# Kernel optimization log

Hardware: AMD Instinct MI355X
Metric: run time of the kernel (lower is better)

## Reference

```python
import jax, jax.numpy as jnp
import numpy as np

B, S, D, F, E = 2, 1024, 1024, 4096, 8

def setup_inputs() -> dict:
    key = jax.random.key(0)
    ks = jax.random.split(key, 4)
    s = 0.02
    return {
        "x": jax.random.normal(ks[0], (B, S, D), dtype=jnp.float32),
        "switch_w": jax.random.normal(ks[1], (D, E), dtype=jnp.float32) * s,
        "switch_b": jnp.zeros((E,), dtype=jnp.float32),
        "w1": jax.random.normal(ks[2], (E, D, F), dtype=jnp.float32) * s,
        "b1": jnp.zeros((E, F), dtype=jnp.float32),
        "w2": jax.random.normal(ks[3], (E, F, D), dtype=jnp.float32) * s,
        "b2": jnp.zeros((E, D), dtype=jnp.float32),
    }

def reference(x, switch_w, switch_b, w1, b1, w2, b2):
    b, s, d = x.shape
    xt = x.reshape(-1, d)                               # [T, D]
    logits = xt @ switch_w + switch_b                   # [T, E]
    route_prob = jax.nn.softmax(logits, axis=-1)        # [T, E]
    route_prob_max = jnp.max(route_prob, axis=-1)       # [T]
    routes = jnp.argmax(route_prob, axis=-1)            # [T] int
    onehot = jax.nn.one_hot(routes, E, dtype=xt.dtype)  # [T, E]
    counts = onehot.sum(axis=0)                         # tokens per expert (float, as in torch new_tensor)

    # top-1 dispatch: run each expert FFN, keep only its tokens via mask (drop_tokens=False -> no capacity drop)
    def body(acc, params):
        W1, B1, W2, B2, mask = params                   # mask: [T]
        y = jax.nn.relu(xt @ W1 + B1) @ W2 + B2         # [T, D]
        return acc + mask[:, None] * y, None

    out, _ = jax.lax.scan(body, jnp.zeros_like(xt), (w1, b1, w2, b2, onehot.T))
    out = out * route_prob_max[:, None]                 # is_scale_prob=True
    final_output = out.reshape(b, s, d)
    return final_output, counts, route_prob.sum(axis=0), 0, route_prob_max
```

## Files before the change

### kernel.cpp

```cpp
#include <hip/hip_runtime.h>
#include <stdint.h>

#define T_TOK 2048
#define D_DIM 1024
#define F_DIM 4096
#define E_NUM 8
#define RPMAX 4096
#define BK 64

typedef __attribute__((ext_vector_type(8))) short bfx8;
typedef __attribute__((ext_vector_type(4))) float fx4;

__device__ __forceinline__ unsigned short f2bf(float f) {
  union { float f; uint32_t u; } v; v.f = f;
  uint32_t u = v.u;
  u += 0x7FFFu + ((u >> 16) & 1u);
  return (unsigned short)(u >> 16);
}

__device__ __forceinline__ void load_lds16(const unsigned short* g, unsigned short* l) {
  __builtin_amdgcn_global_load_lds(
      (const __attribute__((address_space(1))) void*)g,
      (__attribute__((address_space(3))) void*)l, 16, 0, 0);
}

__device__ __forceinline__ uint32_t cvtpk_bf16(float lo, float hi) {
  uint32_t d;
  asm("v_cvt_pk_bf16_f32 %0, %1, %2" : "=v"(d) : "v"(lo), "v"(hi));
  return d;
}

__global__ __launch_bounds__(256) void router_kernel(
    const float* __restrict__ x, const float* __restrict__ sw,
    const float* __restrict__ sb, float* __restrict__ pmax_out,
    int* __restrict__ routes, float* __restrict__ probs,
    unsigned short* __restrict__ xbf) {
  const int wave = threadIdx.x >> 6, lane = threadIdx.x & 63;
  const int t = blockIdx.x * 4 + wave;
  const float* xr = x + (size_t)t * D_DIM;
  float acc[8];
#pragma unroll
  for (int e = 0; e < 8; ++e) acc[e] = 0.f;
#pragma unroll
  for (int i = 0; i < 4; ++i) {
    const int d = i * 256 + lane * 4;
    float4 xv = *(const float4*)(xr + d);
    ushort4 h;
    h.x = f2bf(xv.x); h.y = f2bf(xv.y); h.z = f2bf(xv.z); h.w = f2bf(xv.w);
    *(ushort4*)(xbf + (size_t)t * D_DIM + d) = h;
    const float xs[4] = {xv.x, xv.y, xv.z, xv.w};
#pragma unroll
    for (int j = 0; j < 4; ++j) {
      const float4* swp = (const float4*)(sw + (size_t)(d + j) * 8);
      float4 w0 = swp[0], w1 = swp[1];
      acc[0] += xs[j] * w0.x; acc[1] += xs[j] * w0.y;
      acc[2] += xs[j] * w0.z; acc[3] += xs[j] * w0.w;
      acc[4] += xs[j] * w1.x; acc[5] += xs[j] * w1.y;
      acc[6] += xs[j] * w1.z; acc[7] += xs[j] * w1.w;
    }
  }
#pragma unroll
  for (int e = 0; e < 8; ++e) {
    float v = acc[e];
    for (int o = 32; o > 0; o >>= 1) v += __shfl_down(v, o, 64);
    acc[e] = v;
  }
  if (lane == 0) {
#pragma unroll
    for (int e = 0; e < 8; ++e) acc[e] += sb[e];
    int am = 0; float mx = acc[0];
#pragma unroll
    for (int e = 1; e < 8; ++e) if (acc[e] > mx) { mx = acc[e]; am = e; }
    float p[8]; float s = 0.f;
#pragma unroll
    for (int e = 0; e < 8; ++e) { p[e] = expf(acc[e] - mx); s += p[e]; }
    float inv = 1.0f / s;
    pmax_out[t] = inv;
    routes[t] = am;
#pragma unroll
    for (int e = 0; e < 8; ++e) probs[(size_t)t * 8 + e] = p[e] * inv;
  }
}

__global__ __launch_bounds__(256) void plan_kernel(
    const int* __restrict__ routes, const float* __restrict__ probs,
    int* __restrict__ off, int* __restrict__ perm_out, int* __restrict__ perm_src,
    float* __restrict__ out_counts, float* __restrict__ out_psums,
    float* __restrict__ out_zero) {
  __shared__ int cnt[8];
  __shared__ int cur[8];
  __shared__ int offs[9];
  __shared__ float red[256][8];
  const int tid = threadIdx.x;
  if (tid < 8) cnt[tid] = 0;
  for (int i = tid; i < RPMAX; i += 256) { perm_out[i] = -1; perm_src[i] = 0; }
  __syncthreads();
  float loc[8];
#pragma unroll
  for (int e = 0; e < 8; ++e) loc[e] = 0.f;
  for (int t = tid; t < T_TOK; t += 256) {
    atomicAdd(&cnt[routes[t]], 1);
    const float4* p = (const float4*)(probs + (size_t)t * 8);
    float4 a = p[0], b = p[1];
    loc[0] += a.x; loc[1] += a.y; loc[2] += a.z; loc[3] += a.w;
    loc[4] += b.x; loc[5] += b.y; loc[6] += b.z; loc[7] += b.w;
  }
#pragma unroll
  for (int e = 0; e < 8; ++e) red[tid][e] = loc[e];
  __syncthreads();
  for (int s = 128; s >= 1; s >>= 1) {
    if (tid < s) {
#pragma unroll
      for (int e = 0; e < 8; ++e) red[tid][e] += red[tid + s][e];
    }
    __syncthreads();
  }
  if (tid == 0) {
    int o = 0;
    for (int e = 0; e < 8; ++e) { offs[e] = o; o += ((cnt[e] + 255) >> 8) << 8; }
    offs[8] = o;
    *out_zero = 0.0f;
  }
  __syncthreads();
  if (tid < 9) off[tid] = offs[tid];
  if (tid < 8) {
    cur[tid] = offs[tid];
    out_counts[tid] = (float)cnt[tid];
    out_psums[tid] = red[0][tid];
  }
  __syncthreads();
  for (int t = tid; t < T_TOK; t += 256) {
    int e = routes[t];
    int pos = atomicAdd(&cur[e], 1);
    perm_out[pos] = t;
    perm_src[pos] = t;
  }
}

__global__ __launch_bounds__(256) void gather_kernel(
    const unsigned short* __restrict__ xbf, const int* __restrict__ off,
    const int* __restrict__ perm_src, unsigned short* __restrict__ xg) {
  const int wave = threadIdx.x >> 6, lane = threadIdx.x & 63;
  const int row = blockIdx.x * 4 + wave;
  if (row >= off[8]) return;
  const int tok = perm_src[row];
  const bfx8* s = (const bfx8*)(xbf + (size_t)tok * D_DIM);
  bfx8* d = (bfx8*)(xg + (size_t)row * D_DIM);
  d[lane] = s[lane];
  d[lane + 64] = s[lane + 64];
}

__global__ __launch_bounds__(256) void reduce_kernel(
    const float* __restrict__ P, const int* __restrict__ off,
    const int* __restrict__ perm_out, const float* __restrict__ b2,
    const float* __restrict__ pmax, float* __restrict__ out) {
  const int row = blockIdx.x;
  if (row >= off[8]) return;
  const int tok = perm_out[row];
  if (tok < 0) return;
  int e = 0;
#pragma unroll
  for (int i = 1; i <= 7; ++i) if (row >= off[i]) e = i;
  const int col = threadIdx.x * 4;
  const size_t base = (size_t)row * D_DIM + col;
  float4 p0 = *(const float4*)(P + base);
  float4 p1 = *(const float4*)(P + (size_t)1 * RPMAX * D_DIM + base);
  float4 p2 = *(const float4*)(P + (size_t)2 * RPMAX * D_DIM + base);
  float4 p3 = *(const float4*)(P + (size_t)3 * RPMAX * D_DIM + base);
  float4 bv = *(const float4*)(b2 + (size_t)e * D_DIM + col);
  const float pm = pmax[tok];
  float4 r;
  r.x = (p0.x + p1.x + p2.x + p3.x + bv.x) * pm;
  r.y = (p0.y + p1.y + p2.y + p3.y + bv.y) * pm;
  r.z = (p0.z + p1.z + p2.z + p3.z + bv.z) * pm;
  r.w = (p0.w + p1.w + p2.w + p3.w + bv.w) * pm;
  *(float4*)(out + (size_t)tok * D_DIM + col) = r;
}

template <int K_, int N_>
__global__ __launch_bounds__(512, 4) void gemm1s(
    const unsigned short* __restrict__ A,
    const float* __restrict__ W,
    const float* __restrict__ Bias,
    const int* __restrict__ off,
    unsigned short* __restrict__ Hout) {
  constexpr int BM = 128, BN = 256;
  constexpr int NT = K_ / BK;
  constexpr int FM = 4, FN = 4, GRP = 2;
  constexpr int NBX = N_ / BN;
  __shared__ __align__(16) unsigned short As[BM * 64];
  __shared__ __align__(16) unsigned short Bs[BN * 64];
  const int tid = threadIdx.x;
  const int nby = gridDim.y;
  const int lin = blockIdx.y * NBX + blockIdx.x;
  const int total = NBX * nby;
  const int newlin = (lin & 7) * (total >> 3) + (lin >> 3);
  const int bx = newlin / nby;
  const int by = newlin % nby;
  const int rowbase = by * BM;
  if (rowbase >= off[8]) return;
  int e = 0;
#pragma unroll
  for (int i = 1; i <= 7; ++i) if (rowbase >= off[i]) e = i;
  const int n0 = bx * BN;
  const int wave = tid >> 6, lane = tid & 63;
  const int wm = wave >> 2, wn = wave & 3;
  const float* Wn0 = W + (size_t)e * K_ * N_ + n0;

  const unsigned short* aSrc[2];
#pragma unroll
  for (int c = 0; c < 2; ++c) {
    int ca = (wave * 2 + c) * 64 + lane;
    int row = ca >> 3, slot = ca & 7;
    int sc = slot ^ (row & 7);
    aSrc[c] = A + (size_t)(rowbase + row) * K_ + sc * 8;
  }

  const int nq = lane & 15;
  const int qg = lane >> 4;
  const int kq = (qg & 1) * 4;
  fx4 br[GRP][4];

  fx4 acc[FM][FN];
#pragma unroll
  for (int a = 0; a < FM; ++a)
#pragma unroll
    for (int b = 0; b < FN; ++b) acc[a][b] = (fx4){0.f, 0.f, 0.f, 0.f};

  for (int t = 0; t < NT; ++t) {
    const int kt = t * BK;
#pragma unroll
    for (int c = 0; c < 2; ++c)
      load_lds16(aSrc[c] + kt, As + (wave * 2 + c) * 512);
#pragma unroll
    for (int g = 0; g < GRP; ++g) {
      const int cb = g * 2 + (qg >> 1);
#pragma unroll
      for (int j = 0; j < 4; ++j)
        br[g][j] = *(const fx4*)(Wn0 + (size_t)(kt + wave * 8 + kq + j) * N_ +
                                 cb * 64 + nq * 4);
    }
#pragma unroll
    for (int g = 0; g < GRP; ++g) {
      const int cb = g * 2 + (qg >> 1);
#pragma unroll
      for (int i = 0; i < 4; ++i) {
        const int nl = cb * 64 + nq * 4 + i;
        const int key = ((nl >> 2) + 2 * (nl & 3)) & 7;
        uint32_t d0 = cvtpk_bf16(br[g][0][i], br[g][1][i]);
        uint32_t d1 = cvtpk_bf16(br[g][2][i], br[g][3][i]);
        *(uint2*)(Bs + nl * 64 + (wave ^ key) * 8 + kq) = make_uint2(d0, d1);
      }
    }
    __syncthreads();
#pragma unroll
    for (int kk = 0; kk < 2; ++kk) {
      bfx8 af[FM], bf[FN];
#pragma unroll
      for (int fm = 0; fm < FM; ++fm) {
        int r = wm * 64 + fm * 16 + (lane & 15);
        int c = (kk * 4 + (lane >> 4)) ^ (r & 7);
        af[fm] = *(const bfx8*)(As + r * 64 + c * 8);
      }
#pragma unroll
      for (int fn = 0; fn < FN; ++fn) {
        int nn = wn * 64 + fn * 16 + (lane & 15);
        int key = ((nn >> 2) + 2 * (nn & 3)) & 7;
        int c = (kk * 4 + (lane >> 4)) ^ key;
        bf[fn] = *(const bfx8*)(Bs + nn * 64 + c * 8);
      }
#pragma unroll
      for (int fm = 0; fm < FM; ++fm)
#pragma unroll
        for (int fn = 0; fn < FN; ++fn)
          acc[fm][fn] = __builtin_amdgcn_mfma_f32_16x16x32_bf16(
              af[fm], bf[fn], acc[fm][fn], 0, 0, 0);
    }
    __syncthreads();
  }

  const int colbase = n0 + wn * 64;
#pragma unroll
  for (int fn = 0; fn < FN; ++fn) {
    int colg = colbase + fn * 16 + (lane & 15);
    float bv = Bias[(size_t)e * N_ + colg];
#pragma unroll
    for (int fm = 0; fm < FM; ++fm) {
      int rg = rowbase + wm * 64 + fm * 16 + ((lane >> 4) << 2);
#pragma unroll
      for (int j = 0; j < 4; ++j) {
        float v = fmaxf(acc[fm][fn][j] + bv, 0.f);
        Hout[(size_t)(rg + j) * N_ + colg] = f2bf(v);
      }
    }
  }
}

template <int K_, int N_, int KSPLIT>
__global__ __launch_bounds__(512, 4) void gemm2s(
    const unsigned short* __restrict__ A,
    const float* __restrict__ W,
    const int* __restrict__ off,
    float* __restrict__ Pout) {
  constexpr int BM = 128, BN = 256;
  constexpr int KS = K_ / KSPLIT;
  constexpr int NT = KS / BK;
  constexpr int FM = 4, FN = 4, GRP = 2;
  constexpr int NBX = N_ / BN;
  __shared__ __align__(16) unsigned short As[BM * 64];
  __shared__ __align__(16) unsigned short Bs[BN * 64];
  const int tid = threadIdx.x;
  const int nby = gridDim.y;
  const int lin = (blockIdx.z * nby + blockIdx.y) * NBX + blockIdx.x;
  const int total = NBX * nby * KSPLIT;
  const int newlin = (lin & 7) * (total >> 3) + (lin >> 3);
  const int bx = newlin / (nby * KSPLIT);
  const int rem = newlin % (nby * KSPLIT);
  const int by = rem % nby;
  const int kz = rem / nby;
  const int rowbase = by * BM;
  if (rowbase >= off[8]) return;
  int e = 0;
#pragma unroll
  for (int i = 1; i <= 7; ++i) if (rowbase >= off[i]) e = i;
  const int n0 = bx * BN;
  const int k0base = kz * KS;
  const int wave = tid >> 6, lane = tid & 63;
  const int wm = wave >> 2, wn = wave & 3;
  const float* Wn0 = W + (size_t)e * K_ * N_ + n0;

  const unsigned short* aSrc[2];
#pragma unroll
  for (int c = 0; c < 2; ++c) {
    int ca = (wave * 2 + c) * 64 + lane;
    int row = ca >> 3, slot = ca & 7;
    int sc = slot ^ (row & 7);
    aSrc[c] = A + (size_t)(rowbase + row) * K_ + k0base + sc * 8;
  }

  const int nq = lane & 15;
  const int qg = lane >> 4;
  const int kq = (qg & 1) * 4;
  fx4 br[GRP][4];

  fx4 acc[FM][FN];
#pragma unroll
  for (int a = 0; a < FM; ++a)
#pragma unroll
    for (int b = 0; b < FN; ++b) acc[a][b] = (fx4){0.f, 0.f, 0.f, 0.f};

  for (int t = 0; t < NT; ++t) {
    const int kt = t * BK;
#pragma unroll
    for (int c = 0; c < 2; ++c)
      load_lds16(aSrc[c] + kt, As + (wave * 2 + c) * 512);
#pragma unroll
    for (int g = 0; g < GRP; ++g) {
      const int cb = g * 2 + (qg >> 1);
#pragma unroll
      for (int j = 0; j < 4; ++j)
        br[g][j] = *(const fx4*)(Wn0 + (size_t)(kt + wave * 8 + kq + j) * N_ +
                                 cb * 64 + nq * 4);
    }
#pragma unroll
    for (int g = 0; g < GRP; ++g) {
      const int cb = g * 2 + (qg >> 1);
#pragma unroll
      for (int i = 0; i < 4; ++i) {
        const int nl = cb * 64 + nq * 4 + i;
        const int key = ((nl >> 2) + 2 * (nl & 3)) & 7;
        uint32_t d0 = cvtpk_bf16(br[g][0][i], br[g][1][i]);
        uint32_t d1 = cvtpk_bf16(br[g][2][i], br[g][3][i]);
        *(uint2*)(Bs + nl * 64 + (wave ^ key) * 8 + kq) = make_uint2(d0, d1);
      }
    }
    __syncthreads();
#pragma unroll
    for (int kk = 0; kk < 2; ++kk) {
      bfx8 af[FM], bf[FN];
#pragma unroll
      for (int fm = 0; fm < FM; ++fm) {
        int r = wm * 64 + fm * 16 + (lane & 15);
        int c = (kk * 4 + (lane >> 4)) ^ (r & 7);
        af[fm] = *(const bfx8*)(As + r * 64 + c * 8);
      }
#pragma unroll
      for (int fn = 0; fn < FN; ++fn) {
        int nn = wn * 64 + fn * 16 + (lane & 15);
        int key = ((nn >> 2) + 2 * (nn & 3)) & 7;
        int c = (kk * 4 + (lane >> 4)) ^ key;
        bf[fn] = *(const bfx8*)(Bs + nn * 64 + c * 8);
      }
#pragma unroll
      for (int fm = 0; fm < FM; ++fm)
#pragma unroll
        for (int fn = 0; fn < FN; ++fn)
          acc[fm][fn] = __builtin_amdgcn_mfma_f32_16x16x32_bf16(
              af[fm], bf[fn], acc[fm][fn], 0, 0, 0);
    }
    __syncthreads();
  }

  const int colbase = n0 + wn * 64;
  float* Pk = Pout + (size_t)kz * RPMAX * N_;
#pragma unroll
  for (int fm = 0; fm < FM; ++fm) {
    int rg = rowbase + wm * 64 + fm * 16 + ((lane >> 4) << 2);
#pragma unroll
    for (int j = 0; j < 4; ++j) {
#pragma unroll
      for (int fn = 0; fn < FN; ++fn) {
        int colg = colbase + fn * 16 + (lane & 15);
        Pk[(size_t)(rg + j) * N_ + colg] = acc[fm][fn][j];
      }
    }
  }
}

extern "C" void kernel_launch(void* const* d_in, const int* in_sizes, int n_in,
                              void* d_out, int out_size, void* d_ws, size_t ws_size,
                              hipStream_t stream) {
  const float* x  = (const float*)d_in[0];
  const float* sw = (const float*)d_in[1];
  const float* sb = (const float*)d_in[2];
  const float* w1 = (const float*)d_in[3];
  const float* b1 = (const float*)d_in[4];
  const float* w2 = (const float*)d_in[5];
  const float* b2 = (const float*)d_in[6];
  float* out = (float*)d_out;

  char* ws = (char*)d_ws;
  int*   off      = (int*)(ws + 0);
  int*   routes   = (int*)(ws + 1024);
  int*   perm_out = (int*)(ws + 16384);
  int*   perm_src = (int*)(ws + 32768);
  float* probs    = (float*)(ws + 65536);
  unsigned short* xbf = (unsigned short*)(ws + (1u << 20));
  unsigned short* H   = (unsigned short*)(ws + (8u << 20));
  unsigned short* xg  = (unsigned short*)(ws + (40u << 20));
  float* P            = (float*)(ws + (48u << 20));

  float* out_final  = out;
  float* out_counts = out + 2097152;
  float* out_psums  = out + 2097160;
  float* out_zero   = out + 2097168;
  float* out_pmax   = out + 2097169;

  router_kernel<<<T_TOK / 4, 256, 0, stream>>>(x, sw, sb, out_pmax, routes, probs, xbf);
  plan_kernel<<<1, 256, 0, stream>>>(routes, probs, off, perm_out, perm_src,
                                     out_counts, out_psums, out_zero);
  gather_kernel<<<RPMAX / 4, 256, 0, stream>>>(xbf, off, perm_src, xg);

  gemm1s<D_DIM, F_DIM>
      <<<dim3(F_DIM / 256, RPMAX / 128, 1), 512, 0, stream>>>(
          xg, w1, b1, off, H);
  gemm2s<F_DIM, D_DIM, 4>
      <<<dim3(D_DIM / 256, RPMAX / 128, 4), 512, 0, stream>>>(H, w2, off, P);
  reduce_kernel<<<RPMAX, 256, 0, stream>>>(P, off, perm_out, b2, out_pmax, out_final);
}
```

Measured before the change: 131.3 us.

## Pre-convert W1 to transposed bf16 and stream it via direct LDS loads

Adds a conversion kernel that casts all expert W1 weights to bf16 and transposes them to N-major layout each call. The first expert GEMM then loads B tiles with global_load_lds like A, instead of reading fp32 weights into registers, converting and scattering them into LDS. This removes conversion and register staging from the GEMM inner loop. In exchange it adds a full pass over 128MB of fp32 W1 plus a 64MB bf16 write every call, including experts' rows that the GEMM never reads.

```diff
diff --git a/kernel.cpp b/kernel.cpp
--- a/kernel.cpp
+++ b/kernel.cpp
@@ -148,6 +148,40 @@
   bfx8* d = (bfx8*)(xg + (size_t)row * D_DIM);
   d[lane] = s[lane];
   d[lane + 64] = s[lane + 64];
+}
+
+template <int K_, int N_>
+__global__ __launch_bounds__(256) void conv_kernel(
+    const float* __restrict__ W, unsigned short* __restrict__ WT) {
+  __shared__ unsigned short tile[64][34];
+  const int t = threadIdx.x;
+  const int nbase = blockIdx.x * 32;
+  const int kbase = blockIdx.y * 64;
+  const int e = blockIdx.z;
+  const float* We = W + (size_t)e * K_ * N_;
+  unsigned short* WTe = WT + (size_t)e * N_ * K_;
+  {
+    int kl = t >> 2;
+    int nc = (t & 3) * 8;
+    const float4* src = (const float4*)(We + (size_t)(kbase + kl) * N_ + nbase + nc);
+    float4 a = src[0], b = src[1];
+    unsigned short u[8] = {f2bf(a.x), f2bf(a.y), f2bf(a.z), f2bf(a.w),
+                           f2bf(b.x), f2bf(b.y), f2bf(b.z), f2bf(b.w)};
+#pragma unroll
+    for (int p = 0; p < 4; ++p) {
+      uint32_t pk = (uint32_t)u[2 * p] | ((uint32_t)u[2 * p + 1] << 16);
+      *(uint32_t*)&tile[kl][nc + 2 * p] = pk;
+    }
+  }
+  __syncthreads();
+  {
+    int nl = t >> 3;
+    int kc = (t & 7) * 8;
+    bfx8 v;
+#pragma unroll
+    for (int i = 0; i < 8; ++i) v[i] = (short)tile[kc + i][nl];
+    *(bfx8*)(WTe + (size_t)(nbase + nl) * K_ + kbase + kc) = v;
+  }
 }
 
 __global__ __launch_bounds__(256) void reduce_kernel(
@@ -180,13 +214,13 @@
 template <int K_, int N_>
 __global__ __launch_bounds__(512, 4) void gemm1s(
     const unsigned short* __restrict__ A,
-    const float* __restrict__ W,
+    const unsigned short* __restrict__ WT,
     const float* __restrict__ Bias,
     const int* __restrict__ off,
     unsigned short* __restrict__ Hout) {
   constexpr int BM = 128, BN = 256;
   constexpr int NT = K_ / BK;
-  constexpr int FM = 4, FN = 4, GRP = 2;
+  constexpr int FM = 4, FN = 4;
   constexpr int NBX = N_ / BN;
   __shared__ __align__(16) unsigned short As[BM * 64];
   __shared__ __align__(16) unsigned short Bs[BN * 64];
@@ -205,7 +239,6 @@
   const int n0 = bx * BN;
   const int wave = tid >> 6, lane = tid & 63;
   const int wm = wave >> 2, wn = wave & 3;
-  const float* Wn0 = W + (size_t)e * K_ * N_ + n0;
 
   const unsigned short* aSrc[2];
 #pragma unroll
@@ -215,11 +248,14 @@
     int sc = slot ^ (row & 7);
     aSrc[c] = A + (size_t)(rowbase + row) * K_ + sc * 8;
   }
-
-  const int nq = lane & 15;
-  const int qg = lane >> 4;
-  const int kq = (qg & 1) * 4;
-  fx4 br[GRP][4];
+  const unsigned short* bSrc[4];
+#pragma unroll
+  for (int c = 0; c < 4; ++c) {
+    int cb = (wave * 4 + c) * 64 + lane;
+    int row = cb >> 3, slot = cb & 7;
+    int sc = slot ^ (row & 7);
+    bSrc[c] = WT + ((size_t)e * N_ + (n0 + row)) * (size_t)K_ + sc * 8;
+  }
 
   fx4 acc[FM][FN];
 #pragma unroll
@@ -233,25 +269,8 @@
     for (int c = 0; c < 2; ++c)
       load_lds16(aSrc[c] + kt, As + (wave * 2 + c) * 512);
 #pragma unroll
-    for (int g = 0; g < GRP; ++g) {
-      const int cb = g * 2 + (qg >> 1);
-#pragma unroll
-      for (int j = 0; j < 4; ++j)
-        br[g][j] = *(const fx4*)(Wn0 + (size_t)(kt + wave * 8 + kq + j) * N_ +
-                                 cb * 64 + nq * 4);
-    }
-#pragma unroll
-    for (int g = 0; g < GRP; ++g) {
-      const int cb = g * 2 + (qg >> 1);
-#pragma unroll
-      for (int i = 0; i < 4; ++i) {
-        const int nl = cb * 64 + nq * 4 + i;
-        const int key = ((nl >> 2) + 2 * (nl & 3)) & 7;
-        uint32_t d0 = cvtpk_bf16(br[g][0][i], br[g][1][i]);
-        uint32_t d1 = cvtpk_bf16(br[g][2][i], br[g][3][i]);
-        *(uint2*)(Bs + nl * 64 + (wave ^ key) * 8 + kq) = make_uint2(d0, d1);
-      }
-    }
+    for (int c = 0; c < 4; ++c)
+      load_lds16(bSrc[c] + kt, Bs + (wave * 4 + c) * 512);
     __syncthreads();
 #pragma unroll
     for (int kk = 0; kk < 2; ++kk) {
@@ -265,8 +284,7 @@
 #pragma unroll
       for (int fn = 0; fn < FN; ++fn) {
         int nn = wn * 64 + fn * 16 + (lane & 15);
-        int key = ((nn >> 2) + 2 * (nn & 3)) & 7;
-        int c = (kk * 4 + (lane >> 4)) ^ key;
+        int c = (kk * 4 + (lane >> 4)) ^ (nn & 7);
         bf[fn] = *(const bfx8*)(Bs + nn * 64 + c * 8);
       }
 #pragma unroll
@@ -439,6 +457,7 @@
   unsigned short* H   = (unsigned short*)(ws + (8u << 20));
   unsigned short* xg  = (unsigned short*)(ws + (40u << 20));
   float* P            = (float*)(ws + (48u << 20));
+  unsigned short* WT1 = (unsigned short*)(ws + (112u << 20));
 
   float* out_final  = out;
   float* out_counts = out + 2097152;
@@ -451,9 +470,11 @@
                                      out_counts, out_psums, out_zero);
   gather_kernel<<<RPMAX / 4, 256, 0, stream>>>(xbf, off, perm_src, xg);
 
+  conv_kernel<D_DIM, F_DIM><<<dim3(F_DIM / 32, D_DIM / 64, E_NUM), 256, 0, stream>>>(w1, WT1);
+
   gemm1s<D_DIM, F_DIM>
       <<<dim3(F_DIM / 256, RPMAX / 128, 1), 512, 0, stream>>>(
-          xg, w1, b1, off, H);
+          xg, WT1, b1, off, H);
   gemm2s<F_DIM, D_DIM, 4>
       <<<dim3(D_DIM / 256, RPMAX / 128, 4), 512, 0, stream>>>(H, w2, off, P);
   reduce_kernel<<<RPMAX, 256, 0, stream>>>(P, off, perm_out, b2, out_pmax, out_final);
```

Measured after the change: 159.8 us. +21.7%, slower.

## Compact GEMM grids to live tiles and halve gemm1 N tile width

Applied to the files above, without the earlier changes.

Both expert GEMMs now launch a flat 1D grid and map block IDs only onto live row tiles (from the padded total offset), with the swizzle computed over live tiles. Padded rows no longer create dead blocks and the L2-friendly grouping stays dense. gemm1 also narrows BN from 256 to 128, doubling its tile count for better CU occupancy. The cost is less weight reuse per A tile in gemm1 and more redundant A loads.

```diff
diff --git a/kernel.cpp b/kernel.cpp
--- a/kernel.cpp
+++ b/kernel.cpp
@@ -184,21 +184,22 @@
     const float* __restrict__ Bias,
     const int* __restrict__ off,
     unsigned short* __restrict__ Hout) {
-  constexpr int BM = 128, BN = 256;
+  constexpr int BM = 128, BN = 128;
   constexpr int NT = K_ / BK;
-  constexpr int FM = 4, FN = 4, GRP = 2;
+  constexpr int FM = 4, FN = 2;
   constexpr int NBX = N_ / BN;
   __shared__ __align__(16) unsigned short As[BM * 64];
   __shared__ __align__(16) unsigned short Bs[BN * 64];
   const int tid = threadIdx.x;
-  const int nby = gridDim.y;
-  const int lin = blockIdx.y * NBX + blockIdx.x;
-  const int total = NBX * nby;
-  const int newlin = (lin & 7) * (total >> 3) + (lin >> 3);
-  const int bx = newlin / nby;
-  const int by = newlin % nby;
+  const int bid = blockIdx.x;
+  const int live_by = off[8] >> 7;
+  const int live = live_by * NBX;
+  if (bid >= live) return;
+  const int chunk = live >> 3;
+  const int newlin = (bid & 7) * chunk + (bid >> 3);
+  const int bx = newlin / live_by;
+  const int by = newlin % live_by;
   const int rowbase = by * BM;
-  if (rowbase >= off[8]) return;
   int e = 0;
 #pragma unroll
   for (int i = 1; i <= 7; ++i) if (rowbase >= off[i]) e = i;
@@ -219,7 +220,8 @@
   const int nq = lane & 15;
   const int qg = lane >> 4;
   const int kq = (qg & 1) * 4;
-  fx4 br[GRP][4];
+  const int cb = qg >> 1;
+  fx4 br[4];
 
   fx4 acc[FM][FN];
 #pragma unroll
@@ -233,24 +235,16 @@
     for (int c = 0; c < 2; ++c)
       load_lds16(aSrc[c] + kt, As + (wave * 2 + c) * 512);
 #pragma unroll
-    for (int g = 0; g < GRP; ++g) {
-      const int cb = g * 2 + (qg >> 1);
-#pragma unroll
-      for (int j = 0; j < 4; ++j)
-        br[g][j] = *(const fx4*)(Wn0 + (size_t)(kt + wave * 8 + kq + j) * N_ +
-                                 cb * 64 + nq * 4);
-    }
-#pragma unroll
-    for (int g = 0; g < GRP; ++g) {
-      const int cb = g * 2 + (qg >> 1);
-#pragma unroll
-      for (int i = 0; i < 4; ++i) {
-        const int nl = cb * 64 + nq * 4 + i;
-        const int key = ((nl >> 2) + 2 * (nl & 3)) & 7;
-        uint32_t d0 = cvtpk_bf16(br[g][0][i], br[g][1][i]);
-        uint32_t d1 = cvtpk_bf16(br[g][2][i], br[g][3][i]);
-        *(uint2*)(Bs + nl * 64 + (wave ^ key) * 8 + kq) = make_uint2(d0, d1);
-      }
+    for (int j = 0; j < 4; ++j)
+      br[j] = *(const fx4*)(Wn0 + (size_t)(kt + wave * 8 + kq + j) * N_ +
+                            cb * 64 + nq * 4);
+#pragma unroll
+    for (int i = 0; i < 4; ++i) {
+      const int nl = cb * 64 + nq * 4 + i;
+      const int key = ((nl >> 2) + 2 * (nl & 3)) & 7;
+      uint32_t d0 = cvtpk_bf16(br[0][i], br[1][i]);
+      uint32_t d1 = cvtpk_bf16(br[2][i], br[3][i]);
+      *(uint2*)(Bs + nl * 64 + (wave ^ key) * 8 + kq) = make_uint2(d0, d1);
     }
     __syncthreads();
 #pragma unroll
@@ -264,7 +258,7 @@
       }
 #pragma unroll
       for (int fn = 0; fn < FN; ++fn) {
-        int nn = wn * 64 + fn * 16 + (lane & 15);
+        int nn = wn * 32 + fn * 16 + (lane & 15);
         int key = ((nn >> 2) + 2 * (nn & 3)) & 7;
         int c = (kk * 4 + (lane >> 4)) ^ key;
         bf[fn] = *(const bfx8*)(Bs + nn * 64 + c * 8);
@@ -279,7 +273,7 @@
     __syncthreads();
   }
 
-  const int colbase = n0 + wn * 64;
+  const int colbase = n0 + wn * 32;
 #pragma unroll
   for (int fn = 0; fn < FN; ++fn) {
     int colg = colbase + fn * 16 + (lane & 15);
@@ -310,16 +304,17 @@
   __shared__ __align__(16) unsigned short As[BM * 64];
   __shared__ __align__(16) unsigned short Bs[BN * 64];
   const int tid = threadIdx.x;
-  const int nby = gridDim.y;
-  const int lin = (blockIdx.z * nby + blockIdx.y) * NBX + blockIdx.x;
-  const int total = NBX * nby * KSPLIT;
-  const int newlin = (lin & 7) * (total >> 3) + (lin >> 3);
-  const int bx = newlin / (nby * KSPLIT);
-  const int rem = newlin % (nby * KSPLIT);
-  const int by = rem % nby;
-  const int kz = rem / nby;
+  const int bid = blockIdx.x;
+  const int live_by = off[8] >> 7;
+  const int live = live_by * NBX * KSPLIT;
+  if (bid >= live) return;
+  const int chunk = live >> 3;
+  const int newlin = (bid & 7) * chunk + (bid >> 3);
+  const int bx = newlin / (live_by * KSPLIT);
+  const int rem = newlin % (live_by * KSPLIT);
+  const int by = rem % live_by;
+  const int kz = rem / live_by;
   const int rowbase = by * BM;
-  if (rowbase >= off[8]) return;
   int e = 0;
 #pragma unroll
   for (int i = 1; i <= 7; ++i) if (rowbase >= off[i]) e = i;
@@ -451,10 +446,7 @@
                                      out_counts, out_psums, out_zero);
   gather_kernel<<<RPMAX / 4, 256, 0, stream>>>(xbf, off, perm_src, xg);
 
-  gemm1s<D_DIM, F_DIM>
-      <<<dim3(F_DIM / 256, RPMAX / 128, 1), 512, 0, stream>>>(
-          xg, w1, b1, off, H);
-  gemm2s<F_DIM, D_DIM, 4>
-      <<<dim3(D_DIM / 256, RPMAX / 128, 4), 512, 0, stream>>>(H, w2, off, P);
+  gemm1s<D_DIM, F_DIM><<<1024, 512, 0, stream>>>(xg, w1, b1, off, H);
+  gemm2s<F_DIM, D_DIM, 4><<<512, 512, 0, stream>>>(H, w2, off, P);
   reduce_kernel<<<RPMAX, 256, 0, stream>>>(P, off, perm_out, b2, out_pmax, out_final);
 }
```

Measured after the change: 150.0 us. +14.2%, slower.
